# Kernel tuning notes

Hardware: AMD Instinct MI355X
Metric: run time of the kernel (lower is better)

The kernel has to match this reference:

```python
import jax, jax.numpy as jnp
import numpy as np
from jax import lax

SL, BS, D, H, T = 256, 64, 1024, 512, 17
BN_EPS = 1e-5


def setup_inputs() -> dict:
    key = jax.random.key(0)
    ks = jax.random.split(key, 16)
    k = 1.0 / np.sqrt(H)
    u = lambda kk, shape: jax.random.uniform(kk, shape, jnp.float32, -k, k)
    word_input = jax.random.normal(ks[0], (SL, BS, D), jnp.float32)
    lengths = jax.random.randint(ks[1], (BS,), SL // 2, SL + 1)
    mask = jnp.arange(SL)[:, None] < lengths[None, :]  # (SL, BS), first step all valid
    labels = jax.random.randint(ks[2], (SL, BS), 0, T)
    return dict(
        word_input=word_input, mask=mask, labels=labels,
        w_ih_f=u(ks[3], (4 * H, D)), w_hh_f=u(ks[4], (4 * H, H)),
        b_ih_f=u(ks[5], (4 * H,)), b_hh_f=u(ks[6], (4 * H,)),
        w_ih_b=u(ks[7], (4 * H, D)), w_hh_b=u(ks[8], (4 * H, H)),
        b_ih_b=u(ks[9], (4 * H,)), b_hh_b=u(ks[10], (4 * H,)),
        bn_gamma=jnp.ones((2 * H,), jnp.float32), bn_beta=jnp.zeros((2 * H,), jnp.float32),
        lin_w=u(ks[11], (T, 2 * H)), lin_b=u(ks[12], (T,)),
        crf_start=0.1 * jax.random.normal(ks[13], (T,), jnp.float32),
        crf_end=0.1 * jax.random.normal(ks[14], (T,), jnp.float32),
        crf_trans=0.1 * jax.random.normal(ks[15], (T, T), jnp.float32),
    )


def _lstm_dir(x, w_ih, w_hh, b_ih, b_hh, reverse):
    # x: (SL, BS, D); PyTorch gate order i, f, g, o
    B = x.shape[1]
    h0 = jnp.zeros((B, H), x.dtype)
    xg = jnp.einsum('sbd,gd->sbg', x, w_ih) + b_ih + b_hh  # precompute input projections

    def step(carry, xt):
        h, c = carry
        g = xt + h @ w_hh.T
        i, f, gg, o = jnp.split(g, 4, axis=-1)
        c = jax.nn.sigmoid(f) * c + jax.nn.sigmoid(i) * jnp.tanh(gg)
        h = jax.nn.sigmoid(o) * jnp.tanh(c)
        return (h, c), h

    _, hs = lax.scan(step, (h0, h0), xg, reverse=reverse)
    return hs  # (SL, BS, H)


def _crf_llh(E, y, m, start, end, trans):
    # E: (B, L, T) batch-first emissions; y: (B, L) int; m: (B, L) bool
    B = E.shape[0]
    mf = m.astype(E.dtype)
    b = jnp.arange(B)
    # numerator (gold path score)
    emit = jnp.take_along_axis(E, y[:, :, None], axis=2)[:, :, 0]  # (B, L)
    num = start[y[:, 0]] + emit[:, 0]
    tr = trans[y[:, :-1], y[:, 1:]]  # (B, L-1)
    num = num + jnp.sum(mf[:, 1:] * (tr + emit[:, 1:]), axis=1)
    last = jnp.sum(m.astype(jnp.int32), axis=1) - 1
    num = num + end[y[b, last]]
    # partition function via forward algorithm
    alpha0 = start + E[:, 0]  # (B, T)

    def step(alpha, inp):
        e_t, m_t = inp
        nxt = jax.nn.logsumexp(alpha[:, :, None] + trans[None], axis=1) + e_t
        return jnp.where(m_t[:, None], nxt, alpha), None

    alpha, _ = lax.scan(step, alpha0, (E[:, 1:].transpose(1, 0, 2), m[:, 1:].T))
    Z = jax.nn.logsumexp(alpha + end, axis=1)
    return jnp.sum(num - Z)


def _viterbi(E, m, start, end, trans):
    # E: (B, L, T); m: (B, L) bool -> padded tags (B, L)
    B = E.shape[0]
    b = jnp.arange(B)
    score0 = start + E[:, 0]  # (B, T)

    def fwd(score, inp):
        e_t, m_t = inp
        cand = score[:, :, None] + trans[None]  # (B, T, T)
        best_prev = jnp.argmax(cand, axis=1)  # (B, T)
        best = jnp.max(cand, axis=1) + e_t
        return jnp.where(m_t[:, None], best, score), best_prev

    final, history = lax.scan(fwd, score0, (E[:, 1:].transpose(1, 0, 2), m[:, 1:].T))
    last_tag = jnp.argmax(final + end, axis=1)  # (B,)

    def bwd(tag, inp):
        bp, m_t = inp
        prev = jnp.where(m_t, bp[b, tag], tag)
        return prev, tag

    tag0, tags_rest = lax.scan(bwd, last_tag, (history, m[:, 1:].T), reverse=True)
    tags = jnp.concatenate([tag0[None], tags_rest], axis=0).T  # (B, L)
    return jnp.where(m, tags, 0)


def _forward(word_input, mask, labels, w_ih_f, w_hh_f, b_ih_f, b_hh_f,
             w_ih_b, w_hh_b, b_ih_b, b_hh_b, bn_gamma, bn_beta, lin_w, lin_b,
             crf_start, crf_end, crf_trans):
    hf = _lstm_dir(word_input, w_ih_f, w_hh_f, b_ih_f, b_hh_f, reverse=False)
    hb = _lstm_dir(word_input, w_ih_b, w_hh_b, b_ih_b, b_hh_b, reverse=True)
    lstm_out = jnp.concatenate([hf, hb], axis=-1)  # (SL, BS, 2H)
    x = lstm_out.reshape(-1, 2 * H)
    mean = x.mean(0)
    var = x.var(0)  # biased, as in torch BN training normalization
    xn = (x - mean) / jnp.sqrt(var + BN_EPS) * bn_gamma + bn_beta
    logits = xn @ lin_w.T + lin_b  # (SL*BS, T)
    E = logits.reshape(SL, BS, T).transpose(1, 0, 2)  # batch-first (B, L, T)
    m = mask.T  # (B, L)
    loss = -_crf_llh(E, labels.T, m, crf_start, crf_end, crf_trans)
    preds = _viterbi(E, m, crf_start, crf_end, crf_trans)
    return loss, preds


def reference(word_input, mask, labels, w_ih_f, w_hh_f, b_ih_f, b_hh_f,
              w_ih_b, w_hh_b, b_ih_b, b_hh_b, bn_gamma, bn_beta, lin_w, lin_b,
              crf_start, crf_end, crf_trans):
    return _forward(word_input, mask, labels, w_ih_f, w_hh_f, b_ih_f, b_hh_f,
                    w_ih_b, w_hh_b, b_ih_b, b_hh_b, bn_gamma, bn_beta, lin_w, lin_b,
                    crf_start, crf_end, crf_trans)
```

## Files before the change

kernel.cpp:

```cpp
#include <hip/hip_runtime.h>
#include <hip/hip_bf16.h>
#include <math.h>

#define SL 256
#define BS 64
#define DI 1024
#define HH 512
#define TT 17
#define NR (SL*BS)
#define G4 (4*HH)
#define C2 (2*HH)
#define NBLK 256

__device__ __forceinline__ float sigm(float x) { return 1.f / (1.f + expf(-x)); }

typedef float vfloat4 __attribute__((ext_vector_type(4)));

__device__ __forceinline__ void coh_load4(float4& d, const float* p) {
    asm volatile("global_load_dwordx4 %0, %1, off sc0 sc1" : "=v"(d) : "v"(p) : "memory");
}
__device__ __forceinline__ void coh_load4i(int4& d, const int* p) {
    asm volatile("global_load_dwordx4 %0, %1, off sc0 sc1" : "=v"(d) : "v"(p) : "memory");
}
__device__ __forceinline__ void coh_store4(const float4& d, float* p) {
    vfloat4 t; t.x = d.x; t.y = d.y; t.z = d.z; t.w = d.w;
    asm volatile("global_store_dwordx4 %0, %1, off sc0 sc1" :: "v"(p), "v"(t) : "memory");
}
__device__ __forceinline__ void wait_vm0() { asm volatile("s_waitcnt vmcnt(0)" ::: "memory"); }

__global__ __launch_bounds__(256) void pack_whh_v3(const float* __restrict__ whh,
                                                   float* __restrict__ wp)
{
    const int s = blockIdx.x;
    for (int idx = threadIdx.x; idx < 512 * 12; idx += 256) {
        const int k = idx / 12, c = idx % 12;
        float v = 0.f;
        if (c < 8) {
            const int g = c >> 1, uu = c & 1;
            v = whh[(size_t)(g * 512 + 2 * s + uu) * HH + k];
        }
        wp[(size_t)s * 6144 + idx] = v;
    }
}

__global__ __launch_bounds__(512) void init_flags(int* __restrict__ f)
{
    f[blockIdx.x * 512 + threadIdx.x] = 0;
}

__global__ __launch_bounds__(256) void gemm_xg(
    const float* __restrict__ A,
    const float* __restrict__ W,
    const float* __restrict__ b1,
    const float* __restrict__ b2,
    float* __restrict__ C)
{
    __shared__ float As[16][128];
    __shared__ float Bs[16][128];
    const int tid = threadIdx.x;
    const int m0 = blockIdx.x * 128;
    const int n0 = blockIdx.y * 128;
    const int tm = tid >> 4;
    const int tn = tid & 15;
    const int lr = tid >> 2;
    const int lc = (tid & 3) * 4;

    float acc[8][8];
    #pragma unroll
    for (int i = 0; i < 8; i++)
        #pragma unroll
        for (int j = 0; j < 8; j++) acc[i][j] = 0.f;

    for (int kt = 0; kt < DI; kt += 16) {
        #pragma unroll
        for (int p = 0; p < 2; p++) {
            float4 v = *(const float4*)(A + (size_t)(m0 + p * 64 + lr) * DI + kt + lc);
            As[lc + 0][p * 64 + lr] = v.x;
            As[lc + 1][p * 64 + lr] = v.y;
            As[lc + 2][p * 64 + lr] = v.z;
            As[lc + 3][p * 64 + lr] = v.w;
            float4 w = *(const float4*)(W + (size_t)(n0 + p * 64 + lr) * DI + kt + lc);
            Bs[lc + 0][p * 64 + lr] = w.x;
            Bs[lc + 1][p * 64 + lr] = w.y;
            Bs[lc + 2][p * 64 + lr] = w.z;
            Bs[lc + 3][p * 64 + lr] = w.w;
        }
        __syncthreads();
        #pragma unroll
        for (int kk = 0; kk < 16; kk++) {
            float4 a0 = *(const float4*)&As[kk][tm * 8];
            float4 a1 = *(const float4*)&As[kk][tm * 8 + 4];
            float4 bv0 = *(const float4*)&Bs[kk][tn * 8];
            float4 bv1 = *(const float4*)&Bs[kk][tn * 8 + 4];
            float a[8] = {a0.x, a0.y, a0.z, a0.w, a1.x, a1.y, a1.z, a1.w};
            float b[8] = {bv0.x, bv0.y, bv0.z, bv0.w, bv1.x, bv1.y, bv1.z, bv1.w};
            #pragma unroll
            for (int i = 0; i < 8; i++)
                #pragma unroll
                for (int j = 0; j < 8; j++)
                    acc[i][j] = fmaf(a[i], b[j], acc[i][j]);
        }
        __syncthreads();
    }
    const int g  = n0 >> 9;
    const int u0 = (n0 & 511) + tn * 8;
    const int s0 = u0 >> 1;
    #pragma unroll
    for (int i = 0; i < 8; i++) {
        const int m = m0 + tm * 8 + i;
        const int mt = m >> 6, mb = m & 63;
        #pragma unroll
        for (int sj = 0; sj < 4; sj++) {
            const int n = n0 + tn * 8 + sj * 2;
            float2 v;
            v.x = acc[i][sj * 2 + 0] + b1[n + 0] + b2[n + 0];
            v.y = acc[i][sj * 2 + 1] + b1[n + 1] + b2[n + 1];
            *(float2*)(C + ((((size_t)(s0 + sj) * SL + mt) * BS + mb) << 3) + g * 2) = v;
        }
    }
}

__global__ __launch_bounds__(512, 4) void lstm_flag(
    const float* __restrict__ xg_f, const float* __restrict__ xg_b,
    const float* __restrict__ wp_f, const float* __restrict__ wp_b,
    float* __restrict__ Hf, float* __restrict__ Hb,
    int* __restrict__ flag_f, int* __restrict__ flag_b,
    float* __restrict__ out,
    int dir_base)
{
    __shared__ float w_s[512 * 12];
    __shared__ float hs[128 * 68];
    __shared__ float hpub[128];
    float* const part = hs;
    float* const g_s  = hs + 8 * 572;

    const int dir = dir_base + (blockIdx.x >> 8);
    const int s   = blockIdx.x & 255;
    const float* xg  = dir ? xg_b : xg_f;
    const float* wp  = dir ? wp_b : wp_f;
    float* Hbuf      = dir ? Hb : Hf;
    int*   flag      = dir ? flag_b : flag_f;
    const int reverse = dir;
    const int col_off = dir * HH;

    const int tid = threadIdx.x;
    const int ks  = tid >> 4;
    const int bt  = (tid >> 1) & 7;
    const int ct  = tid & 1;
    const int wv  = tid >> 6;
    const int bb  = tid >> 3;
    const int cc  = tid & 7;

    {
        const float4* src = (const float4*)(wp + (size_t)s * 6144);
        float4* dst = (float4*)w_s;
        for (int i = tid; i < 1536; i += 512) dst[i] = src[i];
    }

    const float* xgs = xg + (size_t)s * (SL * 512);
    float cst = 0.f;
    float4 r[4];
    float4 acc[8];

    for (int step = 0; step < SL; ++step) {
        const int t = reverse ? (SL - 1 - step) : step;
        const float myxg = xgs[t * 512 + tid];

        if (step > 0) {
            if (tid < 64) {
                const int* fp = flag + (step - 1) * NBLK + tid * 4;
                int4 f;
                for (;;) {
                    coh_load4i(f, fp);
                    wait_vm0();
                    if (f.x & f.y & f.z & f.w) break;
                    __builtin_amdgcn_s_sleep(1);
                }
            }
            __syncthreads();

            const float* hsrc = Hbuf + ((step + 1) & 1) * (512 * 64);
            #pragma unroll
            for (int i = 0; i < 4; ++i)
                coh_load4(r[i], hsrc + (size_t)(i * 512 + tid) * 4);

            #pragma unroll
            for (int i = 0; i < 8; ++i) acc[i] = make_float4(0.f, 0.f, 0.f, 0.f);

            for (int kc = 0; kc < 4; ++kc) {
                if (kc) __syncthreads();
                wait_vm0();
                #pragma unroll
                for (int i = 0; i < 4; ++i) {
                    const int idx = i * 512 + tid;
                    const int k = idx >> 4, b4 = (idx & 15) * 4;
                    *(float4*)&hs[k * 68 + b4] = r[i];
                }
                __syncthreads();
                if (kc < 3) {
                    const float* base = hsrc + (size_t)(kc + 1) * 8192;
                    #pragma unroll
                    for (int i = 0; i < 4; ++i)
                        coh_load4(r[i], base + (size_t)(i * 512 + tid) * 4);
                }
                #pragma unroll
                for (int j = 0; j < 4; ++j) {
                    const int kk = ks + 32 * j;
                    const int kg = kc * 128 + kk;
                    const float4 w = *(const float4*)&w_s[kg * 12 + ct * 4];
                    const float* hp = &hs[kk * 68 + 8 * bt];
                    const float2 h01 = *(const float2*)(hp + 0);
                    const float2 h23 = *(const float2*)(hp + 2);
                    const float2 h45 = *(const float2*)(hp + 4);
                    const float2 h67 = *(const float2*)(hp + 6);
                    const float hv[8] = {h01.x, h01.y, h23.x, h23.y, h45.x, h45.y, h67.x, h67.y};
                    #pragma unroll
                    for (int i = 0; i < 8; ++i) {
                        acc[i].x = fmaf(hv[i], w.x, acc[i].x);
                        acc[i].y = fmaf(hv[i], w.y, acc[i].y);
                        acc[i].z = fmaf(hv[i], w.z, acc[i].z);
                        acc[i].w = fmaf(hv[i], w.w, acc[i].w);
                    }
                }
            }
            #pragma unroll
            for (int i = 0; i < 8; ++i) {
                acc[i].x += __shfl_xor(acc[i].x, 16);
                acc[i].y += __shfl_xor(acc[i].y, 16);
                acc[i].z += __shfl_xor(acc[i].z, 16);
                acc[i].w += __shfl_xor(acc[i].w, 16);
                acc[i].x += __shfl_xor(acc[i].x, 32);
                acc[i].y += __shfl_xor(acc[i].y, 32);
                acc[i].z += __shfl_xor(acc[i].z, 32);
                acc[i].w += __shfl_xor(acc[i].w, 32);
            }
            __syncthreads();
            if ((tid & 63) < 16) {
                #pragma unroll
                for (int i = 0; i < 8; ++i)
                    *(float4*)&part[wv * 572 + (8 * bt + i) * 8 + ct * 4 + bt * 8] = acc[i];
            }
            __syncthreads();
        }

        {
            float v = myxg;
            if (step > 0) {
                const int skew = 8 * (tid >> 6);
                #pragma unroll
                for (int w = 0; w < 8; ++w) v += part[w * 572 + tid + skew];
            }
            g_s[cc * 65 + bb] = v;
        }
        __syncthreads();

        if (tid < 128) {
            const int b = tid & 63, uu = tid >> 6;
            const float ig = sigm(g_s[(0 + uu) * 65 + b]);
            const float fg = sigm(g_s[(2 + uu) * 65 + b]);
            const float gg = tanhf(g_s[(4 + uu) * 65 + b]);
            const float og = sigm(g_s[(6 + uu) * 65 + b]);
            cst = fg * cst + ig * gg;
            hpub[tid] = og * tanhf(cst);
        }
        __syncthreads();
        if (tid < 8) {
            const float4 v = *(const float4*)&hpub[tid * 16];
            coh_store4(v, Hbuf + (step & 1) * (512 * 64) + 2 * s * 64 + tid * 16);
            *(float4*)(out + (size_t)(col_off + 2 * s + (tid >> 2)) * NR
                           + (size_t)t * 64 + (tid & 3) * 16) = v;
        }
        if (wv == 0) wait_vm0();
        __syncthreads();
        if (tid == 0)
            __hip_atomic_store(flag + step * NBLK + s, 1,
                               __ATOMIC_RELEASE, __HIP_MEMORY_SCOPE_AGENT);
    }
}

__global__ __launch_bounds__(256) void bn_stats(
    const float* __restrict__ X2, float* __restrict__ mean, float* __restrict__ istd)
{
    const int ch = blockIdx.x, tid = threadIdx.x;
    const float* base = X2 + (size_t)ch * NR;
    __shared__ float red[256];
    float s = 0.f;
    for (int i = tid * 4; i < NR; i += 1024) {
        const float4 v = *(const float4*)(base + i);
        s += v.x + v.y + v.z + v.w;
    }
    red[tid] = s; __syncthreads();
    for (int o = 128; o; o >>= 1) { if (tid < o) red[tid] += red[tid + o]; __syncthreads(); }
    const float mu = red[0] * (1.f / NR);
    __syncthreads();
    float vv = 0.f;
    for (int i = tid * 4; i < NR; i += 1024) {
        const float4 v = *(const float4*)(base + i);
        const float d0 = v.x - mu, d1 = v.y - mu, d2 = v.z - mu, d3 = v.w - mu;
        vv += d0 * d0 + d1 * d1 + d2 * d2 + d3 * d3;
    }
    red[tid] = vv; __syncthreads();
    for (int o = 128; o; o >>= 1) { if (tid < o) red[tid] += red[tid + o]; __syncthreads(); }
    if (tid == 0) { mean[ch] = mu; istd[ch] = rsqrtf(red[0] * (1.f / NR) + 1e-5f); }
}

__global__ void fold_lin(const float* __restrict__ lin_w, const float* __restrict__ lin_b,
                         const float* __restrict__ gamma, const float* __restrict__ beta,
                         const float* __restrict__ mean, const float* __restrict__ istd,
                         float* __restrict__ Wf, float* __restrict__ ct)
{
    const int t = blockIdx.x, tid = threadIdx.x;
    __shared__ float red[256];
    float acc = 0.f;
    for (int cc = tid; cc < C2; cc += 256) {
        const float w = lin_w[t * C2 + cc];
        const float g = gamma[cc] * istd[cc];
        Wf[t * C2 + cc] = w * g;
        acc = fmaf(beta[cc] - mean[cc] * g, w, acc);
    }
    red[tid] = acc; __syncthreads();
    for (int o = 128; o; o >>= 1) { if (tid < o) red[tid] += red[tid + o]; __syncthreads(); }
    if (tid == 0) ct[t] = red[0] + lin_b[t];
}

__global__ __launch_bounds__(256) void emit_logits(
    const float* __restrict__ X2, const float* __restrict__ Wf,
    const float* __restrict__ ct, float* __restrict__ E)
{
    __shared__ float ps[256 * TT];
    const int t = blockIdx.x;
    const int tid = threadIdx.x;
    const int b = tid & 63, p = tid >> 6;
    const float* xb = X2 + (size_t)t * 64 + b;

    float acc[TT];
    #pragma unroll
    for (int k = 0; k < TT; k++) acc[k] = 0.f;

    for (int c0 = p * 256; c0 < p * 256 + 256; c0 += 4) {
        const float x0 = xb[(size_t)(c0 + 0) * NR];
        const float x1 = xb[(size_t)(c0 + 1) * NR];
        const float x2 = xb[(size_t)(c0 + 2) * NR];
        const float x3 = xb[(size_t)(c0 + 3) * NR];
        #pragma unroll
        for (int k = 0; k < TT; k++) {
            const float4 w = *(const float4*)&Wf[k * C2 + c0];
            acc[k] = fmaf(x0, w.x, fmaf(x1, w.y, fmaf(x2, w.z, fmaf(x3, w.w, acc[k]))));
        }
    }
    #pragma unroll
    for (int k = 0; k < TT; k++) ps[tid * TT + k] = acc[k];
    __syncthreads();
    if (tid < 64) {
        float* Er = E + ((size_t)tid * SL + t) * TT;
        #pragma unroll
        for (int k = 0; k < TT; k++) {
            float v = ct[k];
            #pragma unroll
            for (int q = 0; q < 4; q++) v += ps[(q * 64 + tid) * TT + k];
            Er[k] = v;
        }
    }
}

__global__ __launch_bounds__(64) void crf_llh(
    const float* __restrict__ E, const int* __restrict__ mask,
    const int* __restrict__ labels, const float* __restrict__ startv,
    const float* __restrict__ endv, const float* __restrict__ trans,
    float* __restrict__ res)
{
    const int b = blockIdx.x, lane = threadIdx.x;
    __shared__ float tr[TT][TT];
    for (int i = lane; i < TT * TT; i += 64) tr[i / TT][i % TT] = trans[i];
    __syncthreads();
    const float* Eb = E + (size_t)b * SL * TT;
    const int j = (lane < TT) ? lane : 0;

    float alpha = -1e30f;
    if (lane < TT) alpha = startv[lane] + Eb[lane];

    float numacc = 0.f; int len = 0;
    for (int t = lane; t < SL; t += 64) {
        const int mt = mask[t * BS + b];
        len += (mt != 0);
        if (t >= 1 && mt) {
            const int yp = labels[(t - 1) * BS + b];
            const int yt = labels[t * BS + b];
            numacc += tr[yp][yt] + Eb[t * TT + yt];
        }
    }
    for (int off = 32; off; off >>= 1) {
        numacc += __shfl_xor(numacc, off);
        len += __shfl_xor(len, off);
    }

    for (int t = 1; t < SL; ++t) {
        const int mt = mask[t * BS + b];
        if (mt) {
            float av[TT];
            #pragma unroll
            for (int i = 0; i < TT; i++) av[i] = __shfl(alpha, i);
            const float e = (lane < TT) ? Eb[t * TT + lane] : 0.f;
            float mx = -1e30f;
            #pragma unroll
            for (int i = 0; i < TT; i++) mx = fmaxf(mx, av[i] + tr[i][j]);
            float ssum = 0.f;
            #pragma unroll
            for (int i = 0; i < TT; i++) ssum += expf(av[i] + tr[i][j] - mx);
            const float nxt = mx + logf(ssum) + e;
            if (lane < TT) alpha = nxt;
        }
    }
    float v = (lane < TT) ? alpha + endv[lane] : -1e30f;
    float mx = v;
    for (int off = 32; off; off >>= 1) mx = fmaxf(mx, __shfl_xor(mx, off));
    float se = (lane < TT) ? expf(v - mx) : 0.f;
    for (int off = 32; off; off >>= 1) se += __shfl_xor(se, off);
    const float Z = mx + logf(se);

    if (lane == 0) {
        const int y0 = labels[b];
        float num = startv[y0] + Eb[y0] + numacc;
        const int last = len - 1;
        const int yl = labels[last * BS + b];
        num += endv[yl];
        res[b] = num - Z;
    }
}

__global__ __launch_bounds__(64) void loss_reduce(const float* __restrict__ res, float* __restrict__ out)
{
    const int lane = threadIdx.x;
    float v = res[lane];
    for (int off = 32; off; off >>= 1) v += __shfl_xor(v, off);
    if (lane == 0) out[0] = -v;
}

__global__ __launch_bounds__(64) void viterbi(
    const float* __restrict__ E, const int* __restrict__ mask,
    const float* __restrict__ startv, const float* __restrict__ endv,
    const float* __restrict__ trans, float* __restrict__ preds)
{
    const int b = blockIdx.x, lane = threadIdx.x;
    __shared__ float tr[TT][TT];
    __shared__ unsigned char bp[SL][TT];
    for (int i = lane; i < TT * TT; i += 64) tr[i / TT][i % TT] = trans[i];
    __syncthreads();
    const float* Eb = E + (size_t)b * SL * TT;
    const int j = (lane < TT) ? lane : 0;

    float score = (lane < TT) ? startv[lane] + Eb[lane] : -1e30f;
    for (int t = 1; t < SL; ++t) {
        float av[TT];
        #pragma unroll
        for (int i = 0; i < TT; i++) av[i] = __shfl(score, i);
        float best = -1e30f; int bi = 0;
        #pragma unroll
        for (int i = 0; i < TT; i++) {
            const float cand = av[i] + tr[i][j];
            if (cand > best) { best = cand; bi = i; }
        }
        const int mt = mask[t * BS + b];
        if (lane < TT) {
            bp[t][lane] = (unsigned char)bi;
            if (mt) score = best + Eb[t * TT + lane];
        }
    }
    float v = (lane < TT) ? score + endv[lane] : -1e30f;
    float mx = v;
    for (int off = 32; off; off >>= 1) mx = fmaxf(mx, __shfl_xor(mx, off));
    unsigned long long ball = __ballot(v == mx);
    const int last_tag = __ffsll(ball) - 1;
    __syncthreads();

    if (lane == 0) {
        int tag = last_tag;
        float* pb = preds + (size_t)b * SL;
        for (int t = SL - 1; t >= 1; --t) {
            const int mt = mask[t * BS + b];
            pb[t] = mt ? (float)tag : 0.f;
            if (mt) tag = bp[t][tag];
        }
        pb[0] = mask[b] ? (float)tag : 0.f;
    }
}

extern "C" void kernel_launch(void* const* d_in, const int* in_sizes, int n_in,
                              void* d_out, int out_size, void* d_ws, size_t ws_size,
                              hipStream_t stream)
{
    const float* word    = (const float*)d_in[0];
    const int*   mask    = (const int*)  d_in[1];
    const int*   labels  = (const int*)  d_in[2];
    const float* w_ih_f  = (const float*)d_in[3];
    const float* w_hh_f  = (const float*)d_in[4];
    const float* b_ih_f  = (const float*)d_in[5];
    const float* b_hh_f  = (const float*)d_in[6];
    const float* w_ih_b  = (const float*)d_in[7];
    const float* w_hh_b  = (const float*)d_in[8];
    const float* b_ih_b  = (const float*)d_in[9];
    const float* b_hh_b  = (const float*)d_in[10];
    const float* gamma   = (const float*)d_in[11];
    const float* beta    = (const float*)d_in[12];
    const float* lin_w   = (const float*)d_in[13];
    const float* lin_b   = (const float*)d_in[14];
    const float* c_start = (const float*)d_in[15];
    const float* c_end   = (const float*)d_in[16];
    const float* c_trans = (const float*)d_in[17];
    float* out = (float*)d_out;
    (void)in_sizes; (void)n_in; (void)out_size;

    char* ws = (char*)d_ws;
    size_t off = 0;
    auto alloc = [&](size_t bytes) {
        void* p = ws + off;
        off += (bytes + 255) & ~(size_t)255;
        return p;
    };
    float* XG_F  = (float*)alloc((size_t)NR * G4 * 4);
    float* WPK_F = (float*)alloc((size_t)256 * 6144 * 4);
    float* WPK_B = (float*)alloc((size_t)256 * 6144 * 4);
    float* LOUT  = (float*)alloc((size_t)NR * C2 * 4);
    float* HB_F  = (float*)alloc((size_t)2 * 512 * 64 * 4);
    float* HB_B  = (float*)alloc((size_t)2 * 512 * 64 * 4);
    int*   FLAGS = (int*)  alloc((size_t)2 * SL * NBLK * 4);
    float* MEAN  = (float*)alloc(C2 * 4);
    float* ISTD  = (float*)alloc(C2 * 4);
    float* WF    = (float*)alloc(TT * C2 * 4);
    float* CT    = (float*)alloc(TT * 4);
    float* Ebuf  = (float*)alloc((size_t)BS * SL * TT * 4);
    float* RES   = (float*)alloc(BS * 4);
    float* XG_B  = (float*)alloc((size_t)NR * G4 * 4);
    const bool merged = (ws_size >= off);
    if (!merged) XG_B = XG_F;

    init_flags<<<256, 512, 0, stream>>>(FLAGS);
    pack_whh_v3<<<256, 256, 0, stream>>>(w_hh_f, WPK_F);
    pack_whh_v3<<<256, 256, 0, stream>>>(w_hh_b, WPK_B);

    if (merged) {
        gemm_xg<<<dim3(NR / 128, G4 / 128), 256, 0, stream>>>(word, w_ih_f, b_ih_f, b_hh_f, XG_F);
        gemm_xg<<<dim3(NR / 128, G4 / 128), 256, 0, stream>>>(word, w_ih_b, b_ih_b, b_hh_b, XG_B);
        lstm_flag<<<2 * NBLK, 512, 0, stream>>>(XG_F, XG_B, WPK_F, WPK_B, HB_F, HB_B,
                                                FLAGS, FLAGS + SL * NBLK, LOUT, 0);
    } else {
        gemm_xg<<<dim3(NR / 128, G4 / 128), 256, 0, stream>>>(word, w_ih_f, b_ih_f, b_hh_f, XG_F);
        lstm_flag<<<NBLK, 512, 0, stream>>>(XG_F, XG_B, WPK_F, WPK_B, HB_F, HB_B,
                                            FLAGS, FLAGS + SL * NBLK, LOUT, 0);
        gemm_xg<<<dim3(NR / 128, G4 / 128), 256, 0, stream>>>(word, w_ih_b, b_ih_b, b_hh_b, XG_F);
        lstm_flag<<<NBLK, 512, 0, stream>>>(XG_F, XG_B, WPK_F, WPK_B, HB_F, HB_B,
                                            FLAGS, FLAGS + SL * NBLK, LOUT, 1);
    }

    bn_stats<<<C2, 256, 0, stream>>>(LOUT, MEAN, ISTD);
    fold_lin<<<TT, 256, 0, stream>>>(lin_w, lin_b, gamma, beta, MEAN, ISTD, WF, CT);
    emit_logits<<<SL, 256, 0, stream>>>(LOUT, WF, CT, Ebuf);

    crf_llh<<<BS, 64, 0, stream>>>(Ebuf, mask, labels, c_start, c_end, c_trans, RES);
    loss_reduce<<<1, 64, 0, stream>>>(RES, out);
    viterbi<<<BS, 64, 0, stream>>>(Ebuf, mask, c_start, c_end, c_trans, out + 1);
}
```

Before: 9.484 ms.

## Halve LSTM recurrence blocks, each block computing four hidden units instead of two

The persistent flag-synchronised LSTM kernel now runs 128 blocks per direction instead of 256. Each block owns four hidden units and their 16 gate columns, so the packed weight slice and the xg layout are widened to match. The aim is to cut per-step grid synchronisation cost: half as many flags to poll and fewer blocks contending, with each block doing twice the FMA work. In exchange the per-block recurrence compute doubles, LDS use grows, and occupancy drops to 2 blocks per CU, which may lengthen the per-step critical path.

```diff
diff --git a/kernel.cpp b/kernel.cpp
--- a/kernel.cpp
+++ b/kernel.cpp
@@ -10,7 +10,7 @@
 #define NR (SL*BS)
 #define G4 (4*HH)
 #define C2 (2*HH)
-#define NBLK 256
+#define NBLK 128
 
 __device__ __forceinline__ float sigm(float x) { return 1.f / (1.f + expf(-x)); }
 
@@ -32,14 +32,14 @@
                                                    float* __restrict__ wp)
 {
     const int s = blockIdx.x;
-    for (int idx = threadIdx.x; idx < 512 * 12; idx += 256) {
-        const int k = idx / 12, c = idx % 12;
+    for (int idx = threadIdx.x; idx < 512 * 24; idx += 256) {
+        const int k = idx / 24, c = idx % 24;
         float v = 0.f;
-        if (c < 8) {
-            const int g = c >> 1, uu = c & 1;
-            v = whh[(size_t)(g * 512 + 2 * s + uu) * HH + k];
-        }
-        wp[(size_t)s * 6144 + idx] = v;
+        if (c < 16) {
+            const int g = c >> 2, uu = c & 3;
+            v = whh[(size_t)(g * 512 + 4 * s + uu) * HH + k];
+        }
+        wp[(size_t)s * 12288 + idx] = v;
     }
 }
 
@@ -104,7 +104,7 @@
     }
     const int g  = n0 >> 9;
     const int u0 = (n0 & 511) + tn * 8;
-    const int s0 = u0 >> 1;
+    const int s0 = u0 >> 2;
     #pragma unroll
     for (int i = 0; i < 8; i++) {
         const int m = m0 + tm * 8 + i;
@@ -115,12 +115,13 @@
             float2 v;
             v.x = acc[i][sj * 2 + 0] + b1[n + 0] + b2[n + 0];
             v.y = acc[i][sj * 2 + 1] + b1[n + 1] + b2[n + 1];
-            *(float2*)(C + ((((size_t)(s0 + sj) * SL + mt) * BS + mb) << 3) + g * 2) = v;
-        }
-    }
-}
-
-__global__ __launch_bounds__(512, 4) void lstm_flag(
+            *(float2*)(C + ((((size_t)(s0 + (sj >> 1)) * SL + mt) * BS + mb) << 4)
+                         + g * 4 + 2 * (sj & 1)) = v;
+        }
+    }
+}
+
+__global__ __launch_bounds__(512, 2) void lstm_flag(
     const float* __restrict__ xg_f, const float* __restrict__ xg_b,
     const float* __restrict__ wp_f, const float* __restrict__ wp_b,
     float* __restrict__ Hf, float* __restrict__ Hb,
@@ -128,14 +129,14 @@
     float* __restrict__ out,
     int dir_base)
 {
-    __shared__ float w_s[512 * 12];
+    __shared__ float w_s[512 * 24];
     __shared__ float hs[128 * 68];
-    __shared__ float hpub[128];
+    __shared__ float g_s[16 * 65];
+    __shared__ float hpub[256];
     float* const part = hs;
-    float* const g_s  = hs + 8 * 572;
-
-    const int dir = dir_base + (blockIdx.x >> 8);
-    const int s   = blockIdx.x & 255;
+
+    const int dir = dir_base + (blockIdx.x >> 7);
+    const int s   = blockIdx.x & 127;
     const float* xg  = dir ? xg_b : xg_f;
     const float* wp  = dir ? wp_b : wp_f;
     float* Hbuf      = dir ? Hb : Hf;
@@ -148,26 +149,25 @@
     const int bt  = (tid >> 1) & 7;
     const int ct  = tid & 1;
     const int wv  = tid >> 6;
-    const int bb  = tid >> 3;
-    const int cc  = tid & 7;
 
     {
-        const float4* src = (const float4*)(wp + (size_t)s * 6144);
+        const float4* src = (const float4*)(wp + (size_t)s * 12288);
         float4* dst = (float4*)w_s;
-        for (int i = tid; i < 1536; i += 512) dst[i] = src[i];
-    }
-
-    const float* xgs = xg + (size_t)s * (SL * 512);
+        for (int i = tid; i < 3072; i += 512) dst[i] = src[i];
+    }
+
+    const float* xgs = xg + (size_t)s * (SL * 1024);
     float cst = 0.f;
     float4 r[4];
-    float4 acc[8];
+    float4 acc[8][2];
 
     for (int step = 0; step < SL; ++step) {
         const int t = reverse ? (SL - 1 - step) : step;
-        const float myxg = xgs[t * 512 + tid];
+        const float myxg0 = xgs[t * 1024 + tid];
+        const float myxg1 = xgs[t * 1024 + 512 + tid];
 
         if (step > 0) {
-            if (tid < 64) {
+            if (tid < 32) {
                 const int* fp = flag + (step - 1) * NBLK + tid * 4;
                 int4 f;
                 for (;;) {
@@ -185,7 +185,10 @@
                 coh_load4(r[i], hsrc + (size_t)(i * 512 + tid) * 4);
 
             #pragma unroll
-            for (int i = 0; i < 8; ++i) acc[i] = make_float4(0.f, 0.f, 0.f, 0.f);
+            for (int i = 0; i < 8; ++i) {
+                acc[i][0] = make_float4(0.f, 0.f, 0.f, 0.f);
+                acc[i][1] = make_float4(0.f, 0.f, 0.f, 0.f);
+            }
 
             for (int kc = 0; kc < 4; ++kc) {
                 if (kc) __syncthreads();
@@ -207,7 +210,8 @@
                 for (int j = 0; j < 4; ++j) {
                     const int kk = ks + 32 * j;
                     const int kg = kc * 128 + kk;
-                    const float4 w = *(const float4*)&w_s[kg * 12 + ct * 4];
+                    const float4 w0 = *(const float4*)&w_s[kg * 24 + ct * 8];
+                    const float4 w1 = *(const float4*)&w_s[kg * 24 + ct * 8 + 4];
                     const float* hp = &hs[kk * 68 + 8 * bt];
                     const float2 h01 = *(const float2*)(hp + 0);
                     const float2 h23 = *(const float2*)(hp + 2);
@@ -216,58 +220,76 @@
                     const float hv[8] = {h01.x, h01.y, h23.x, h23.y, h45.x, h45.y, h67.x, h67.y};
                     #pragma unroll
                     for (int i = 0; i < 8; ++i) {
-                        acc[i].x = fmaf(hv[i], w.x, acc[i].x);
-                        acc[i].y = fmaf(hv[i], w.y, acc[i].y);
-                        acc[i].z = fmaf(hv[i], w.z, acc[i].z);
-                        acc[i].w = fmaf(hv[i], w.w, acc[i].w);
+                        acc[i][0].x = fmaf(hv[i], w0.x, acc[i][0].x);
+                        acc[i][0].y = fmaf(hv[i], w0.y, acc[i][0].y);
+                        acc[i][0].z = fmaf(hv[i], w0.z, acc[i][0].z);
+                        acc[i][0].w = fmaf(hv[i], w0.w, acc[i][0].w);
+                        acc[i][1].x = fmaf(hv[i], w1.x, acc[i][1].x);
+                        acc[i][1].y = fmaf(hv[i], w1.y, acc[i][1].y);
+                        acc[i][1].z = fmaf(hv[i], w1.z, acc[i][1].z);
+                        acc[i][1].w = fmaf(hv[i], w1.w, acc[i][1].w);
                     }
                 }
             }
             #pragma unroll
-            for (int i = 0; i < 8; ++i) {
-                acc[i].x += __shfl_xor(acc[i].x, 16);
-                acc[i].y += __shfl_xor(acc[i].y, 16);
-                acc[i].z += __shfl_xor(acc[i].z, 16);
-                acc[i].w += __shfl_xor(acc[i].w, 16);
-                acc[i].x += __shfl_xor(acc[i].x, 32);
-                acc[i].y += __shfl_xor(acc[i].y, 32);
-                acc[i].z += __shfl_xor(acc[i].z, 32);
-                acc[i].w += __shfl_xor(acc[i].w, 32);
-            }
+            for (int i = 0; i < 8; ++i)
+                #pragma unroll
+                for (int p = 0; p < 2; ++p) {
+                    acc[i][p].x += __shfl_xor(acc[i][p].x, 16);
+                    acc[i][p].y += __shfl_xor(acc[i][p].y, 16);
+                    acc[i][p].z += __shfl_xor(acc[i][p].z, 16);
+                    acc[i][p].w += __shfl_xor(acc[i][p].w, 16);
+                    acc[i][p].x += __shfl_xor(acc[i][p].x, 32);
+                    acc[i][p].y += __shfl_xor(acc[i][p].y, 32);
+                    acc[i][p].z += __shfl_xor(acc[i][p].z, 32);
+                    acc[i][p].w += __shfl_xor(acc[i][p].w, 32);
+                }
             __syncthreads();
             if ((tid & 63) < 16) {
                 #pragma unroll
-                for (int i = 0; i < 8; ++i)
-                    *(float4*)&part[wv * 572 + (8 * bt + i) * 8 + ct * 4 + bt * 8] = acc[i];
+                for (int i = 0; i < 8; ++i) {
+                    const int base = wv * 1088 + (8 * bt + i) * 16 + ct * 8 + bt * 8;
+                    *(float4*)&part[base + 0] = acc[i][0];
+                    *(float4*)&part[base + 4] = acc[i][1];
+                }
             }
             __syncthreads();
         }
 
         {
-            float v = myxg;
+            float v0 = myxg0, v1 = myxg1;
             if (step > 0) {
-                const int skew = 8 * (tid >> 6);
+                const int gA = tid, gB = tid + 512;
+                const int iA = gA + 8 * (gA >> 7);
+                const int iB = gB + 8 * (gB >> 7);
                 #pragma unroll
-                for (int w = 0; w < 8; ++w) v += part[w * 572 + tid + skew];
+                for (int w = 0; w < 8; ++w) {
+                    v0 += part[w * 1088 + iA];
+                    v1 += part[w * 1088 + iB];
+                }
             }
-            g_s[cc * 65 + bb] = v;
+            g_s[(tid & 15) * 65 + (tid >> 4)] = v0;
+            {
+                const int gB = tid + 512;
+                g_s[(gB & 15) * 65 + (gB >> 4)] = v1;
+            }
         }
         __syncthreads();
 
-        if (tid < 128) {
+        if (tid < 256) {
             const int b = tid & 63, uu = tid >> 6;
-            const float ig = sigm(g_s[(0 + uu) * 65 + b]);
-            const float fg = sigm(g_s[(2 + uu) * 65 + b]);
-            const float gg = tanhf(g_s[(4 + uu) * 65 + b]);
-            const float og = sigm(g_s[(6 + uu) * 65 + b]);
+            const float ig = sigm(g_s[(0  + uu) * 65 + b]);
+            const float fg = sigm(g_s[(4  + uu) * 65 + b]);
+            const float gg = tanhf(g_s[(8  + uu) * 65 + b]);
+            const float og = sigm(g_s[(12 + uu) * 65 + b]);
             cst = fg * cst + ig * gg;
             hpub[tid] = og * tanhf(cst);
         }
         __syncthreads();
-        if (tid < 8) {
+        if (tid < 16) {
             const float4 v = *(const float4*)&hpub[tid * 16];
-            coh_store4(v, Hbuf + (step & 1) * (512 * 64) + 2 * s * 64 + tid * 16);
-            *(float4*)(out + (size_t)(col_off + 2 * s + (tid >> 2)) * NR
+            coh_store4(v, Hbuf + (step & 1) * (512 * 64) + s * 256 + tid * 16);
+            *(float4*)(out + (size_t)(col_off + 4 * s + (tid >> 2)) * NR
                            + (size_t)t * 64 + (tid & 3) * 16) = v;
         }
         if (wv == 0) wait_vm0();
@@ -518,8 +540,8 @@
         return p;
     };
     float* XG_F  = (float*)alloc((size_t)NR * G4 * 4);
-    float* WPK_F = (float*)alloc((size_t)256 * 6144 * 4);
-    float* WPK_B = (float*)alloc((size_t)256 * 6144 * 4);
+    float* WPK_F = (float*)alloc((size_t)128 * 12288 * 4);
+    float* WPK_B = (float*)alloc((size_t)128 * 12288 * 4);
     float* LOUT  = (float*)alloc((size_t)NR * C2 * 4);
     float* HB_F  = (float*)alloc((size_t)2 * 512 * 64 * 4);
     float* HB_B  = (float*)alloc((size_t)2 * 512 * 64 * 4);
@@ -534,9 +556,9 @@
     const bool merged = (ws_size >= off);
     if (!merged) XG_B = XG_F;
 
-    init_flags<<<256, 512, 0, stream>>>(FLAGS);
-    pack_whh_v3<<<256, 256, 0, stream>>>(w_hh_f, WPK_F);
-    pack_whh_v3<<<256, 256, 0, stream>>>(w_hh_b, WPK_B);
+    init_flags<<<128, 512, 0, stream>>>(FLAGS);
+    pack_whh_v3<<<128, 256, 0, stream>>>(w_hh_f, WPK_F);
+    pack_whh_v3<<<128, 256, 0, stream>>>(w_hh_b, WPK_B);
 
     if (merged) {
         gemm_xg<<<dim3(NR / 128, G4 / 128), 256, 0, stream>>>(word, w_ih_f, b_ih_f, b_hh_f, XG_F);
```

Result: no change. 9.514 ms (+0.3%).
